# Optimization experiments

Hardware: AMD Instinct MI355X
Metric: run time of the kernel (lower is better)

The kernel has to match this reference:

```python
import jax, jax.numpy as jnp
import numpy as np
import math

HIDDEN = 1024
NUM_LAYERS = 24
INIT_RANGE = 0.02


def setup_inputs() -> dict:
    key = jax.random.key(0)
    k1, k2 = jax.random.split(key)
    B, S, H = 4, 4096, HIDDEN
    hidden_states = jax.random.normal(k1, (B, S, H), dtype=jnp.float32)
    std = INIT_RANGE / math.sqrt(2.0 * NUM_LAYERS * H)
    # queries weight: [H, H], applied as F.linear => x @ W^T
    W_q = jax.random.normal(k2, (H, H), dtype=jnp.float32) * std
    return {"hidden_states": hidden_states, "W_q": W_q}


def reference(hidden_states, W_q):
    # queries = F.linear(x, W) = x @ W^T          [B, S, H]
    q = jnp.einsum('bsh,oh->bso', hidden_states, W_q)
    # pre_attn = Q @ K^T where K = x             [B, S, S]
    pre_attn = jnp.einsum('bso,bto->bst', q, hidden_states)
    # attention = pre_attn @ V where V = x       [B, S, H]
    attention = jnp.einsum('bst,bth->bsh', pre_attn, hidden_states)
    return attention
```

## Files before the change

kernel.cpp:

```cpp
#include <hip/hip_runtime.h>
#include <hip/hip_bf16.h>
#include <stdint.h>

#define H_DIM 1024
#define S_DIM 4096
#define B_DIM 4

typedef __bf16 bf16x8 __attribute__((ext_vector_type(8)));
typedef float f32x4 __attribute__((ext_vector_type(4)));
typedef unsigned short u16x4 __attribute__((ext_vector_type(4)));
typedef unsigned short u16x8 __attribute__((ext_vector_type(8)));

__device__ __forceinline__ unsigned short f2bf(float f) {
    union { float f; uint32_t u; } v; v.f = f;
    uint32_t u = v.u;
    uint32_t r = (u + 0x7FFFu + ((u >> 16) & 1u)) >> 16;
    return (unsigned short)r;
}
__device__ __forceinline__ float bf2f(unsigned short u) {
    union { uint32_t u; float f; } v; v.u = (uint32_t)u << 16; return v.f;
}

__device__ __forceinline__ void gate_vmcnt0() {
    __builtin_amdgcn_sched_barrier(0);
    asm volatile("s_waitcnt vmcnt(0)");
    __builtin_amdgcn_sched_barrier(0);
}
__device__ __forceinline__ void gate_lgkm0() {
    asm volatile("s_waitcnt lgkmcnt(0)");
    __builtin_amdgcn_sched_barrier(0);
}

template <int IMM>
__device__ __forceinline__ bf16x8 ds_read_b128_imm(unsigned addr) {
    bf16x8 r;
    asm volatile("ds_read_b128 %0, %1 offset:%2"
                 : "=v"(r) : "v"(addr), "i"(IMM));
    return r;
}

__global__ __launch_bounds__(256)
void cast_x_kernel(const float* __restrict__ X,
                   unsigned short* __restrict__ Xb,
                   unsigned short* __restrict__ XT) {
    __shared__ float tile[64][65];
    const int b  = blockIdx.z;
    const int h0 = blockIdx.x * 64;
    const int s0 = blockIdx.y * 64;
    const int tx = threadIdx.x;
    const int ty = threadIdx.y;
#pragma unroll
    for (int j = 0; j < 4; ++j) {
        int s = ty + 16 * j;
        f32x4 v = *(const f32x4*)&X[((size_t)b * S_DIM + s0 + s) * H_DIM + h0 + tx * 4];
        u16x4 o;
#pragma unroll
        for (int k = 0; k < 4; ++k) {
            tile[s][tx * 4 + k] = v[k];
            o[k] = f2bf(v[k]);
        }
        *(u16x4*)&Xb[((size_t)b * S_DIM + s0 + s) * H_DIM + h0 + tx * 4] = o;
    }
    __syncthreads();
#pragma unroll
    for (int j = 0; j < 4; ++j) {
        int hh = ty + 16 * j;
        u16x4 o;
#pragma unroll
        for (int k = 0; k < 4; ++k)
            o[k] = f2bf(tile[tx * 4 + k][hh]);
        *(u16x4*)&XT[((size_t)b * H_DIM + h0 + hh) * S_DIM + s0 + tx * 4] = o;
    }
}

__global__ void cast_w_kernel(const float* __restrict__ W,
                              unsigned short* __restrict__ WT) {
    __shared__ float tile[32][33];
    const int b0 = blockIdx.x * 32;
    const int o0 = blockIdx.y * 32;
    const int tx = threadIdx.x;
    const int ty = threadIdx.y;
#pragma unroll
    for (int i = 0; i < 4; ++i) {
        int o = ty + 8 * i;
        tile[o][tx] = W[(size_t)(o0 + o) * H_DIM + b0 + tx];
    }
    __syncthreads();
#pragma unroll
    for (int i = 0; i < 4; ++i) {
        int bb = ty + 8 * i;
        WT[(size_t)(b0 + bb) * H_DIM + o0 + tx] = f2bf(tile[tx][bb]);
    }
}

template <int NSPLIT>
__global__ void reduce_cast_u16_kernel(const unsigned short* __restrict__ P,
                                       unsigned short* __restrict__ Out,
                                       size_t sSplit) {
    size_t i = ((size_t)blockIdx.x * blockDim.x + threadIdx.x) * 8;
    float s[8] = {0.f, 0.f, 0.f, 0.f, 0.f, 0.f, 0.f, 0.f};
#pragma unroll
    for (int sp = 0; sp < NSPLIT; ++sp) {
        u16x8 u = *(const u16x8*)&P[(size_t)sp * sSplit + i];
#pragma unroll
        for (int k = 0; k < 8; ++k) s[k] += bf2f(u[k]);
    }
    u16x8 o;
#pragma unroll
    for (int k = 0; k < 8; ++k) o[k] = f2bf(s[k]);
    *(u16x8*)&Out[i] = o;
}

template <typename OutT, int NSPLIT>
__global__ __launch_bounds__(512, 4)
void gemm_r9_kernel(const unsigned short* __restrict__ A,
                    const unsigned short* __restrict__ Bt,
                    OutT* __restrict__ C,
                    int K, int lda, int ldb, int ldc,
                    size_t sA, size_t sB, size_t sC, size_t sSplit) {
    extern __shared__ char smem_raw[];

    const int tid  = threadIdx.x;
    const int w    = tid >> 6;
    const int lane = tid & 63;
    const int wm   = w & 3;
    const int wn   = w >> 2;
    const int q    = lane >> 4;
    const int col  = lane & 15;

    const int tileM = blockIdx.x * 256;
    const int tileN = blockIdx.y * 128;
    const int bz   = blockIdx.z / NSPLIT;
    const int sp   = blockIdx.z % NSPLIT;
    const int Ksub = K / NSPLIT;
    const int T    = Ksub >> 5;

    const unsigned short* Ab = A + sA * bz + (size_t)sp * Ksub;
    const unsigned short* Bb = Bt + sB * bz + (size_t)sp * Ksub;

    auto lds3 = (__attribute__((address_space(3))) char*)&smem_raw[0];
    const unsigned ldsBase = (unsigned)(size_t)lds3;

    const int slot = q ^ ((col >> 1) & 3);
    const unsigned aBase = ldsBase + (unsigned)(wm * 4096 + col * 64 + slot * 16);
    const unsigned bBase = ldsBase + 16384u + (unsigned)(wn * 4096 + col * 64 + slot * 16);

    const int lrow = lane >> 2;
    const int koff = ((lane & 3) ^ ((lane >> 3) & 3)) * 8;
    const unsigned short* pA[2];
    unsigned dA[2];
#pragma unroll
    for (int j = 0; j < 2; ++j) {
        int g = 2 * w + j;
        pA[j] = Ab + (size_t)(tileM + g * 16 + lrow) * lda + koff;
        dA[j] = (unsigned)(g * 1024);
    }
    const unsigned short* pB = Bb + (size_t)(tileN + w * 16 + lrow) * ldb + koff;
    const unsigned dB = 16384u + (unsigned)(w * 1024);

    auto stage = [&](int tgt) {
        const unsigned bo = (unsigned)(tgt & 1) * 24576u;
#pragma unroll
        for (int j = 0; j < 2; ++j)
            __builtin_amdgcn_global_load_lds(
                (const __attribute__((address_space(1))) void*)(pA[j] + tgt * 32),
                (__attribute__((address_space(3))) void*)(lds3 + bo + dA[j]),
                16, 0, 0);
        __builtin_amdgcn_global_load_lds(
            (const __attribute__((address_space(1))) void*)(pB + tgt * 32),
            (__attribute__((address_space(3))) void*)(lds3 + bo + dB),
            16, 0, 0);
    };

    f32x4 acc[4][4];
#pragma unroll
    for (int r = 0; r < 4; ++r)
#pragma unroll
        for (int c = 0; c < 4; ++c)
            acc[r][c] = (f32x4){0.f, 0.f, 0.f, 0.f};

    stage(0);

    for (int n = 0; n < T; ++n) {
        gate_vmcnt0();
        __builtin_amdgcn_s_barrier();
        if (n + 1 < T) stage(n + 1);

        const unsigned aAddr = aBase + (unsigned)((n & 1) * 24576);
        const unsigned bAddr = bBase + (unsigned)((n & 1) * 24576);
        bf16x8 av[4], bv[4];
        av[0] = ds_read_b128_imm<0>(aAddr);
        av[1] = ds_read_b128_imm<1024>(aAddr);
        av[2] = ds_read_b128_imm<2048>(aAddr);
        av[3] = ds_read_b128_imm<3072>(aAddr);
        bv[0] = ds_read_b128_imm<0>(bAddr);
        bv[1] = ds_read_b128_imm<1024>(bAddr);
        bv[2] = ds_read_b128_imm<2048>(bAddr);
        bv[3] = ds_read_b128_imm<3072>(bAddr);
        gate_lgkm0();
        __builtin_amdgcn_s_setprio(1);
#pragma unroll
        for (int mf = 0; mf < 4; ++mf)
#pragma unroll
            for (int nf = 0; nf < 4; ++nf)
                acc[mf][nf] = __builtin_amdgcn_mfma_f32_16x16x32_bf16(
                    av[mf], bv[nf], acc[mf][nf], 0, 0, 0);
        __builtin_amdgcn_s_setprio(0);
    }

    OutT* Cb = C + sC * bz + sSplit * sp;
    __syncthreads();
    float* lws = (float*)(smem_raw) + (size_t)w * 1088;
    const int lr = lane >> 4;
    const int lc = lane & 15;
#pragma unroll
    for (int mf = 0; mf < 4; ++mf) {
#pragma unroll
        for (int nf = 0; nf < 4; ++nf)
#pragma unroll
            for (int v = 0; v < 4; ++v)
                lws[(q * 4 + v) * 68 + nf * 16 + col] = acc[mf][nf][v];
#pragma unroll
        for (int p = 0; p < 4; ++p) {
            f32x4 t = *(const f32x4*)&lws[(p * 4 + lr) * 68 + lc * 4];
            int row  = tileM + wm * 64 + mf * 16 + p * 4 + lr;
            int colg = tileN + wn * 64 + lc * 4;
            if constexpr (sizeof(OutT) == 2) {
                u16x4 u;
                u[0] = f2bf(t[0]); u[1] = f2bf(t[1]);
                u[2] = f2bf(t[2]); u[3] = f2bf(t[3]);
                *(u16x4*)&Cb[(size_t)row * ldc + colg] = u;
            } else {
                *(f32x4*)&Cb[(size_t)row * ldc + colg] = t;
            }
        }
    }
}

extern "C" void kernel_launch(void* const* d_in, const int* in_sizes, int n_in,
                              void* d_out, int out_size, void* d_ws, size_t ws_size,
                              hipStream_t stream) {
    const float* X = (const float*)d_in[0];
    const float* W = (const float*)d_in[1];
    float* out = (float*)d_out;

    char* ws = (char*)d_ws;
    unsigned short* Xb = (unsigned short*)(ws);
    unsigned short* XT = (unsigned short*)(ws + 33554432);
    unsigned short* WT = (unsigned short*)(ws + 67108864);
    unsigned short* G  = (unsigned short*)(ws + 69206016);
    unsigned short* MT = (unsigned short*)(ws + 77594624);
    unsigned short* Gpart  = (unsigned short*)(ws + 85983232);
    unsigned short* MTpart = (unsigned short*)(ws + 85983232);

    const size_t sBH = (size_t)B_DIM * H_DIM * H_DIM;

    cast_x_kernel<<<dim3(H_DIM / 64, S_DIM / 64, B_DIM), dim3(16, 16), 0, stream>>>(X, Xb, XT);
    cast_w_kernel<<<dim3(H_DIM / 32, H_DIM / 32, 1), dim3(32, 8), 0, stream>>>(W, WT);

    gemm_r9_kernel<unsigned short, 4><<<dim3(4, 8, B_DIM * 4), 512, 49152, stream>>>(
        XT, XT, Gpart, S_DIM, S_DIM, S_DIM, H_DIM,
        (size_t)H_DIM * S_DIM, (size_t)H_DIM * S_DIM, (size_t)H_DIM * H_DIM, sBH);
    reduce_cast_u16_kernel<4><<<dim3(sBH / 8 / 256), 256, 0, stream>>>(Gpart, G, sBH);

    gemm_r9_kernel<unsigned short, 4><<<dim3(4, 8, B_DIM * 4), 512, 49152, stream>>>(
        G, WT, MTpart, H_DIM, H_DIM, H_DIM, H_DIM,
        (size_t)H_DIM * H_DIM, (size_t)0, (size_t)H_DIM * H_DIM, sBH);
    reduce_cast_u16_kernel<4><<<dim3(sBH / 8 / 256), 256, 0, stream>>>(MTpart, MT, sBH);

    gemm_r9_kernel<float, 1><<<dim3(S_DIM / 256, H_DIM / 128, B_DIM), 512, 49152, stream>>>(
        Xb, MT, out, H_DIM, H_DIM, H_DIM, H_DIM,
        (size_t)S_DIM * H_DIM, (size_t)H_DIM * H_DIM, (size_t)S_DIM * H_DIM, 0);
}
```

Before: 235.0 us.

## Enlarge GEMM tile to 256x256 with 4-stage LDS pipeline

The GEMM kernel tile grows from 256x128 to 256x256, with each wave computing 128x64 (8x4 MFMA fragments). The double buffer becomes a 4-deep ring of 32KB LDS stages (128KB total), kept three loads ahead using partial vmcnt waits. The aim is more operand reuse per global byte and hiding global-load latency. In exchange, occupancy drops to one block per CU, register pressure rises and the grid shrinks to fewer blocks (for example 256 for the first two GEMMs), which may underfill the 256 CUs.

```diff
diff --git a/kernel.cpp b/kernel.cpp
--- a/kernel.cpp
+++ b/kernel.cpp
@@ -21,6 +21,16 @@
     union { uint32_t u; float f; } v; v.u = (uint32_t)u << 16; return v.f;
 }
 
+__device__ __forceinline__ void gate_vmcnt8() {
+    __builtin_amdgcn_sched_barrier(0);
+    asm volatile("s_waitcnt vmcnt(8)");
+    __builtin_amdgcn_sched_barrier(0);
+}
+__device__ __forceinline__ void gate_vmcnt4() {
+    __builtin_amdgcn_sched_barrier(0);
+    asm volatile("s_waitcnt vmcnt(4)");
+    __builtin_amdgcn_sched_barrier(0);
+}
 __device__ __forceinline__ void gate_vmcnt0() {
     __builtin_amdgcn_sched_barrier(0);
     asm volatile("s_waitcnt vmcnt(0)");
@@ -112,24 +122,24 @@
 }
 
 template <typename OutT, int NSPLIT>
-__global__ __launch_bounds__(512, 4)
-void gemm_r9_kernel(const unsigned short* __restrict__ A,
-                    const unsigned short* __restrict__ Bt,
-                    OutT* __restrict__ C,
-                    int K, int lda, int ldb, int ldc,
-                    size_t sA, size_t sB, size_t sC, size_t sSplit) {
+__global__ __launch_bounds__(512, 2)
+void gemm_d10_kernel(const unsigned short* __restrict__ A,
+                     const unsigned short* __restrict__ Bt,
+                     OutT* __restrict__ C,
+                     int K, int lda, int ldb, int ldc,
+                     size_t sA, size_t sB, size_t sC, size_t sSplit) {
     extern __shared__ char smem_raw[];
 
     const int tid  = threadIdx.x;
     const int w    = tid >> 6;
     const int lane = tid & 63;
-    const int wm   = w & 3;
-    const int wn   = w >> 2;
+    const int wm   = w & 1;
+    const int wn   = w >> 1;
     const int q    = lane >> 4;
     const int col  = lane & 15;
 
     const int tileM = blockIdx.x * 256;
-    const int tileN = blockIdx.y * 128;
+    const int tileN = blockIdx.y * 256;
     const int bz   = blockIdx.z / NSPLIT;
     const int sp   = blockIdx.z % NSPLIT;
     const int Ksub = K / NSPLIT;
@@ -142,57 +152,66 @@
     const unsigned ldsBase = (unsigned)(size_t)lds3;
 
     const int slot = q ^ ((col >> 1) & 3);
-    const unsigned aBase = ldsBase + (unsigned)(wm * 4096 + col * 64 + slot * 16);
+    const unsigned aBase = ldsBase + (unsigned)(wm * 8192 + col * 64 + slot * 16);
     const unsigned bBase = ldsBase + 16384u + (unsigned)(wn * 4096 + col * 64 + slot * 16);
 
     const int lrow = lane >> 2;
     const int koff = ((lane & 3) ^ ((lane >> 3) & 3)) * 8;
     const unsigned short* pA[2];
-    unsigned dA[2];
+    const unsigned short* pB[2];
+    unsigned dR[2];
 #pragma unroll
     for (int j = 0; j < 2; ++j) {
         int g = 2 * w + j;
         pA[j] = Ab + (size_t)(tileM + g * 16 + lrow) * lda + koff;
-        dA[j] = (unsigned)(g * 1024);
-    }
-    const unsigned short* pB = Bb + (size_t)(tileN + w * 16 + lrow) * ldb + koff;
-    const unsigned dB = 16384u + (unsigned)(w * 1024);
-
+        pB[j] = Bb + (size_t)(tileN + g * 16 + lrow) * ldb + koff;
+        dR[j] = (unsigned)(g * 1024);
+    }
     auto stage = [&](int tgt) {
-        const unsigned bo = (unsigned)(tgt & 1) * 24576u;
+        const unsigned bo = (unsigned)(tgt & 3) * 32768u;
 #pragma unroll
         for (int j = 0; j < 2; ++j)
             __builtin_amdgcn_global_load_lds(
                 (const __attribute__((address_space(1))) void*)(pA[j] + tgt * 32),
-                (__attribute__((address_space(3))) void*)(lds3 + bo + dA[j]),
+                (__attribute__((address_space(3))) void*)(lds3 + bo + dR[j]),
                 16, 0, 0);
-        __builtin_amdgcn_global_load_lds(
-            (const __attribute__((address_space(1))) void*)(pB + tgt * 32),
-            (__attribute__((address_space(3))) void*)(lds3 + bo + dB),
-            16, 0, 0);
+#pragma unroll
+        for (int j = 0; j < 2; ++j)
+            __builtin_amdgcn_global_load_lds(
+                (const __attribute__((address_space(1))) void*)(pB[j] + tgt * 32),
+                (__attribute__((address_space(3))) void*)(lds3 + bo + 16384u + dR[j]),
+                16, 0, 0);
     };
 
-    f32x4 acc[4][4];
-#pragma unroll
-    for (int r = 0; r < 4; ++r)
+    f32x4 acc[8][4];
+#pragma unroll
+    for (int r = 0; r < 8; ++r)
 #pragma unroll
         for (int c = 0; c < 4; ++c)
             acc[r][c] = (f32x4){0.f, 0.f, 0.f, 0.f};
 
     stage(0);
+    if (T > 1) stage(1);
+    if (T > 2) stage(2);
 
     for (int n = 0; n < T; ++n) {
-        gate_vmcnt0();
+        if (n + 2 < T)      gate_vmcnt8();
+        else if (n + 1 < T) gate_vmcnt4();
+        else                gate_vmcnt0();
         __builtin_amdgcn_s_barrier();
-        if (n + 1 < T) stage(n + 1);
-
-        const unsigned aAddr = aBase + (unsigned)((n & 1) * 24576);
-        const unsigned bAddr = bBase + (unsigned)((n & 1) * 24576);
-        bf16x8 av[4], bv[4];
+        if (n + 3 < T) stage(n + 3);
+
+        const unsigned aAddr = aBase + (unsigned)((n & 3) << 15);
+        const unsigned bAddr = bBase + (unsigned)((n & 3) << 15);
+        bf16x8 av[8], bv[4];
         av[0] = ds_read_b128_imm<0>(aAddr);
         av[1] = ds_read_b128_imm<1024>(aAddr);
         av[2] = ds_read_b128_imm<2048>(aAddr);
         av[3] = ds_read_b128_imm<3072>(aAddr);
+        av[4] = ds_read_b128_imm<4096>(aAddr);
+        av[5] = ds_read_b128_imm<5120>(aAddr);
+        av[6] = ds_read_b128_imm<6144>(aAddr);
+        av[7] = ds_read_b128_imm<7168>(aAddr);
         bv[0] = ds_read_b128_imm<0>(bAddr);
         bv[1] = ds_read_b128_imm<1024>(bAddr);
         bv[2] = ds_read_b128_imm<2048>(bAddr);
@@ -200,7 +219,7 @@
         gate_lgkm0();
         __builtin_amdgcn_s_setprio(1);
 #pragma unroll
-        for (int mf = 0; mf < 4; ++mf)
+        for (int mf = 0; mf < 8; ++mf)
 #pragma unroll
             for (int nf = 0; nf < 4; ++nf)
                 acc[mf][nf] = __builtin_amdgcn_mfma_f32_16x16x32_bf16(
@@ -214,7 +233,7 @@
     const int lr = lane >> 4;
     const int lc = lane & 15;
 #pragma unroll
-    for (int mf = 0; mf < 4; ++mf) {
+    for (int mf = 0; mf < 8; ++mf) {
 #pragma unroll
         for (int nf = 0; nf < 4; ++nf)
 #pragma unroll
@@ -223,7 +242,7 @@
 #pragma unroll
         for (int p = 0; p < 4; ++p) {
             f32x4 t = *(const f32x4*)&lws[(p * 4 + lr) * 68 + lc * 4];
-            int row  = tileM + wm * 64 + mf * 16 + p * 4 + lr;
+            int row  = tileM + wm * 128 + mf * 16 + p * 4 + lr;
             int colg = tileN + wn * 64 + lc * 4;
             if constexpr (sizeof(OutT) == 2) {
                 u16x4 u;
@@ -258,17 +277,17 @@
     cast_x_kernel<<<dim3(H_DIM / 64, S_DIM / 64, B_DIM), dim3(16, 16), 0, stream>>>(X, Xb, XT);
     cast_w_kernel<<<dim3(H_DIM / 32, H_DIM / 32, 1), dim3(32, 8), 0, stream>>>(W, WT);
 
-    gemm_r9_kernel<unsigned short, 4><<<dim3(4, 8, B_DIM * 4), 512, 49152, stream>>>(
+    gemm_d10_kernel<unsigned short, 4><<<dim3(4, 4, B_DIM * 4), 512, 131072, stream>>>(
         XT, XT, Gpart, S_DIM, S_DIM, S_DIM, H_DIM,
         (size_t)H_DIM * S_DIM, (size_t)H_DIM * S_DIM, (size_t)H_DIM * H_DIM, sBH);
     reduce_cast_u16_kernel<4><<<dim3(sBH / 8 / 256), 256, 0, stream>>>(Gpart, G, sBH);
 
-    gemm_r9_kernel<unsigned short, 4><<<dim3(4, 8, B_DIM * 4), 512, 49152, stream>>>(
+    gemm_d10_kernel<unsigned short, 4><<<dim3(4, 4, B_DIM * 4), 512, 131072, stream>>>(
         G, WT, MTpart, H_DIM, H_DIM, H_DIM, H_DIM,
         (size_t)H_DIM * H_DIM, (size_t)0, (size_t)H_DIM * H_DIM, sBH);
     reduce_cast_u16_kernel<4><<<dim3(sBH / 8 / 256), 256, 0, stream>>>(MTpart, MT, sBH);
 
-    gemm_r9_kernel<float, 1><<<dim3(S_DIM / 256, H_DIM / 128, B_DIM), 512, 49152, stream>>>(
+    gemm_d10_kernel<float, 1><<<dim3(S_DIM / 256, H_DIM / 256, B_DIM), 512, 131072, stream>>>(
         Xb, MT, out, H_DIM, H_DIM, H_DIM, H_DIM,
         (size_t)S_DIM * H_DIM, (size_t)H_DIM * H_DIM, (size_t)S_DIM * H_DIM, 0);
 }
```

Result: no change. 231.9 us (-1.3%).
